# Kernel tuning notes

Hardware: AMD Instinct MI355X
Metric: run time of the kernel (lower is better)

The kernel has to match this reference:

```python
import math
import jax, jax.numpy as jnp
import numpy as np

DIM = 2048
HEAD_DIM = 64
N_HEADS = DIM // HEAD_DIM
BATCH = 4
SEQ = 1025  # 32*32 axial positions + 1 zero position
EPS = 1e-6


def make_theta(head_dim=HEAD_DIM, h=32, w=32):
    # freqs: geometric from pi to 10*pi, head_dim//4 of them
    n_freqs = head_dim // 4
    freqs = jnp.exp(jnp.linspace(math.log(math.pi), math.log(10 * math.pi), n_freqs))
    hp = jnp.linspace(-1.0, 1.0, h + 1)
    wp = jnp.linspace(-1.0, 1.0, w + 1)
    hp = (hp[:-1] + hp[1:]) / 2
    wp = (wp[:-1] + wp[1:]) / 2
    pos = jnp.stack(jnp.meshgrid(hp, wp, indexing='ij'), axis=-1).reshape(h * w, 2)
    pos = jnp.concatenate([jnp.zeros((1, 2)), pos], axis=0)  # [1025, 2]
    theta_h = pos[:, 0:1] * freqs  # [S, n_freqs]
    theta_w = pos[:, 1:2] * freqs
    return jnp.concatenate([theta_h, theta_w], axis=-1)  # [S, head_dim//2]


def rms_norm(x, scale, eps=EPS):
    mean_sq = jnp.mean(jnp.square(x.astype(jnp.float32)), axis=-1, keepdims=True)
    s = scale.astype(jnp.float32) * jax.lax.rsqrt(mean_sq + eps)
    return (x * s.astype(x.dtype)).astype(x.dtype)


def apply_rotary(x, theta):
    # x: [B, H, S, D], theta: [S, d] with 2*d <= D
    d = theta.shape[-1]
    x1, x2, x3 = x[..., :d], x[..., d:2 * d], x[..., 2 * d:]
    cos, sin = jnp.cos(theta), jnp.sin(theta)  # broadcast over B, H
    y1 = x1 * cos - x2 * sin
    y2 = x2 * cos + x1 * sin
    return jnp.concatenate([y1, y2, x3], axis=-1)


def setup_inputs() -> dict:
    key = jax.random.key(0)
    k1, k2, k3 = jax.random.split(key, 3)
    x = jax.random.normal(k1, (BATCH, SEQ, DIM), dtype=jnp.float32)
    scale = jnp.ones((DIM,), dtype=jnp.float32)
    w_qkv = jax.random.normal(k2, (3 * DIM, DIM), dtype=jnp.float32) * 0.02
    w_out = jax.random.normal(k3, (DIM, DIM), dtype=jnp.float32) * 0.02
    return {"x": x, "scale": scale, "w_qkv": w_qkv, "w_out": w_out}


def reference(x, scale, w_qkv, w_out):
    B, S, _ = x.shape
    skip = x
    h = rms_norm(x, scale)
    qkv = h @ w_qkv.T  # [B, S, 3*DIM]
    qkv = qkv.reshape(B, S, 3, N_HEADS, HEAD_DIM)
    qkv = jnp.transpose(qkv, (0, 3, 2, 1, 4))  # [B, H, 3, S, D]
    q, k, v = qkv[:, :, 0], qkv[:, :, 1], qkv[:, :, 2]
    theta = make_theta()[:S]
    q = apply_rotary(q, theta)
    k = apply_rotary(k, theta)
    scores = jnp.einsum('bhqd,bhkd->bhqk', q, k) / math.sqrt(HEAD_DIM)
    causal = jnp.tril(jnp.ones((S, S), dtype=bool))
    scores = jnp.where(causal, scores, jnp.finfo(scores.dtype).min)
    attn = jax.nn.softmax(scores, axis=-1)
    o = jnp.einsum('bhqk,bhkd->bhqd', attn, v)  # [B, H, S, D]
    o = jnp.transpose(o, (0, 2, 1, 3)).reshape(B, S, DIM)
    return o @ w_out.T + skip
```

## Files before the change

### kernel.cpp

```cpp
#include <hip/hip_runtime.h>
#include <hip/hip_bf16.h>
#include <cstdint>

#define SEQ   1025
#define SPAD  1088
#define DIM   2048
#define NQKV  6144
#define MROWS 4100
#define MPAD  4352
#define NH    32

typedef __attribute__((ext_vector_type(8))) short bf16x8;
typedef __attribute__((ext_vector_type(4))) short bf16x4;
typedef __attribute__((ext_vector_type(4))) float f32x4;

#define MFMA16x16(A,B,C) __builtin_amdgcn_mfma_f32_16x16x32_bf16(A,B,C,0,0,0)

static __device__ __forceinline__ float bf2f(short s) {
    union { unsigned int u; float f; } v;
    v.u = ((unsigned int)(unsigned short)s) << 16;
    return v.f;
}
static __device__ __forceinline__ short f2bf(float f) {
    union { float f; unsigned int u; } v; v.f = f;
    unsigned int r = v.u + 0x7fffu + ((v.u >> 16) & 1u);
    return (short)(r >> 16);
}

typedef __attribute__((address_space(1))) unsigned int u32g;
typedef __attribute__((address_space(3))) unsigned int u32l;
static __device__ __forceinline__ void gld_lds16(void* lds, const void* g) {
    __builtin_amdgcn_global_load_lds((const u32g*)(uintptr_t)g,
                                     (u32l*)(uintptr_t)lds, 16, 0, 0);
}

#define SBX() __builtin_amdgcn_sched_barrier(0)
#define PRIO(x) __builtin_amdgcn_s_setprio(x)

__global__ __launch_bounds__(256) void trig_k(float* __restrict__ cosT, float* __restrict__ sinT) {
    int i = blockIdx.x * 256 + threadIdx.x;
    if (i >= SEQ * 16) return;
    int s = i >> 4, f = i & 15;
    float ph = 0.f, pw = 0.f;
    if (s > 0) {
        int p = s - 1;
        ph = -1.f + ((p >> 5) + 0.5f) * 0.0625f;
        pw = -1.f + ((p & 31) + 0.5f) * 0.0625f;
    }
    double fr = 3.141592653589793 * exp((double)f * 0.15350567286626973);
    float th = (float)(ph * fr), tw = (float)(pw * fr);
    cosT[s*32 + f]      = cosf(th);
    sinT[s*32 + f]      = sinf(th);
    cosT[s*32 + 16 + f] = cosf(tw);
    sinT[s*32 + 16 + f] = sinf(tw);
}

__global__ __launch_bounds__(256) void rmsnorm_k(const float* __restrict__ x,
                                                 const float* __restrict__ sc,
                                                 short* __restrict__ h) {
    int row = blockIdx.x, t = threadIdx.x;
    short* hr = h + (size_t)row * DIM;
    if (row >= MROWS) {
        bf16x8 z = {};
        *(bf16x8*)(hr + t*8) = z;
        return;
    }
    const float4* xr = (const float4*)(x + (size_t)row * DIM);
    float4 a = xr[2*t], b = xr[2*t+1];
    float ss = a.x*a.x + a.y*a.y + a.z*a.z + a.w*a.w
             + b.x*b.x + b.y*b.y + b.z*b.z + b.w*b.w;
    #pragma unroll
    for (int off = 32; off; off >>= 1) ss += __shfl_xor(ss, off, 64);
    __shared__ float red[4];
    if ((t & 63) == 0) red[t >> 6] = ss;
    __syncthreads();
    float ms = (red[0]+red[1]+red[2]+red[3]) * (1.0f/2048.0f);
    float inv = rsqrtf(ms + 1e-6f);
    const float4* sr = (const float4*)sc;
    float4 s0 = sr[2*t], s1 = sr[2*t+1];
    bf16x8 o;
    o[0]=f2bf(a.x*(s0.x*inv)); o[1]=f2bf(a.y*(s0.y*inv));
    o[2]=f2bf(a.z*(s0.z*inv)); o[3]=f2bf(a.w*(s0.w*inv));
    o[4]=f2bf(b.x*(s1.x*inv)); o[5]=f2bf(b.y*(s1.y*inv));
    o[6]=f2bf(b.z*(s1.z*inv)); o[7]=f2bf(b.w*(s1.w*inv));
    *(bf16x8*)(hr + t*8) = o;
}

__global__ __launch_bounds__(256) void conv_k(const float* __restrict__ in, short* __restrict__ o, int n4) {
    int i = blockIdx.x * 256 + threadIdx.x;
    if (i >= n4) return;
    float4 v = ((const float4*)in)[i];
    bf16x4 r = { f2bf(v.x), f2bf(v.y), f2bf(v.z), f2bf(v.w) };
    *(bf16x4*)(o + (size_t)i*4) = r;
}

__global__ __launch_bounds__(512, 2) void gemm8p(const short* __restrict__ A,
                                                 const short* __restrict__ B,
                                                 short* __restrict__ C,
                                                 int N, int K, int nbm) {
    extern __shared__ char smem[];
    const int nwg = gridDim.x;
    const int cpx = nwg >> 3;
    const int bid = blockIdx.x;
    const int sid = (bid & 7) * cpx + (bid >> 3);
    const int bm = sid % nbm;
    const int bn = sid / nbm;

    const int t = threadIdx.x, w = t >> 6, l = t & 63;
    const int lr = l & 15, lg = l >> 4;
    const int wr = w >> 2, wc = w & 3;

    const short* Ab = A + (size_t)bm * 256 * K;
    const short* Bb = B + (size_t)bn * 256 * K;

    const int srow = t >> 3;
    const int scol = (((t & 7) ^ (srow & 7)) << 3);

    const int cs0 = (lg * 16) ^ ((lr & 7) << 4);
    const int cs1 = (64 + lg * 16) ^ ((lr & 7) << 4);
    const int aRowB = (wr * 128 + lr) * 128;
    const int bRowB = (wc * 64 + lr) * 128;

    f32x4 acc[8][4] = {};
    bf16x8 rA[4][2], rB[4][2];

#define STAGE8(kt, bb) do {                                                   \
    const int k0_ = (kt) * 64;                                                \
    _Pragma("unroll")                                                         \
    for (int c = 0; c < 4; ++c) {                                             \
        gld_lds16(smem + (bb)*65536 + c*8192 + (w<<10),                       \
                  Ab + (size_t)(c*64 + srow) * K + k0_ + scol);               \
        gld_lds16(smem + (bb)*65536 + 32768 + c*8192 + (w<<10),               \
                  Bb + (size_t)(c*64 + srow) * K + k0_ + scol);               \
    }                                                                         \
} while (0)

#define READ_A8(bb, h) do {                                                   \
    const char* p_ = smem + (bb)*65536 + aRowB + (h)*8192;                    \
    _Pragma("unroll")                                                         \
    for (int am = 0; am < 4; ++am) {                                          \
        rA[am][0] = *(const bf16x8*)(p_ + am*2048 + cs0);                     \
        rA[am][1] = *(const bf16x8*)(p_ + am*2048 + cs1);                     \
    }                                                                         \
} while (0)

#define READ_B4(bb, np) do {                                                  \
    const char* p_ = smem + (bb)*65536 + 32768 + bRowB + (np)*4096;           \
    _Pragma("unroll")                                                         \
    for (int nn = 0; nn < 2; ++nn) {                                          \
        rB[(np)*2+nn][0] = *(const bf16x8*)(p_ + nn*2048 + cs0);              \
        rB[(np)*2+nn][1] = *(const bf16x8*)(p_ + nn*2048 + cs1);              \
    }                                                                         \
} while (0)

#define MF_Q(h, nh) do {                                                      \
    _Pragma("unroll")                                                         \
    for (int am = 0; am < 4; ++am)                                            \
    _Pragma("unroll")                                                         \
    for (int nn = 0; nn < 2; ++nn) {                                          \
        acc[(h)*4+am][(nh)*2+nn] =                                            \
            MFMA16x16(rA[am][0], rB[(nh)*2+nn][0], acc[(h)*4+am][(nh)*2+nn]); \
        acc[(h)*4+am][(nh)*2+nn] =                                            \
            MFMA16x16(rA[am][1], rB[(nh)*2+nn][1], acc[(h)*4+am][(nh)*2+nn]); \
    }                                                                         \
} while (0)

#define PH_COMPUTE(h, nh) do {                                                \
    SBX(); __builtin_amdgcn_s_barrier();                                      \
    asm volatile("s_waitcnt lgkmcnt(0)" ::: "memory"); SBX();                 \
    PRIO(1); MF_Q(h, nh); PRIO(0); SBX();                                     \
    __builtin_amdgcn_s_barrier(); SBX();                                      \
} while (0)

    STAGE8(0, 0);
    STAGE8(1, 1);
    asm volatile("s_waitcnt vmcnt(8)" ::: "memory"); SBX();
    __builtin_amdgcn_s_barrier(); SBX();

    const int NT2 = K / 128;
    for (int it = 0; it < NT2; ++it) {
        const bool more = (it < NT2 - 1);
        READ_A8(0, 0); READ_B4(0, 0); PH_COMPUTE(0, 0);
        READ_B4(0, 1);                PH_COMPUTE(0, 1);
        READ_A8(0, 1);                PH_COMPUTE(1, 1);
        if (more) STAGE8(2*it + 2, 0);
        SBX(); __builtin_amdgcn_s_barrier(); SBX();
        PRIO(1); MF_Q(1, 0); PRIO(0); SBX();
        if (more) { asm volatile("s_waitcnt vmcnt(8)" ::: "memory"); }
        else      { asm volatile("s_waitcnt vmcnt(0)" ::: "memory"); }
        SBX(); __builtin_amdgcn_s_barrier(); SBX();
        READ_A8(1, 0); READ_B4(1, 0); PH_COMPUTE(0, 0);
        READ_B4(1, 1);                PH_COMPUTE(0, 1);
        READ_A8(1, 1);                PH_COMPUTE(1, 1);
        if (more) STAGE8(2*it + 3, 1);
        SBX(); __builtin_amdgcn_s_barrier(); SBX();
        PRIO(1); MF_Q(1, 0); PRIO(0); SBX();
        if (more) { asm volatile("s_waitcnt vmcnt(8)" ::: "memory"); SBX(); }
        __builtin_amdgcn_s_barrier(); SBX();
    }

    #pragma unroll
    for (int m = 0; m < 8; ++m) {
        const int row0 = bm*256 + wr*128 + m*16 + lg*4;
        #pragma unroll
        for (int n = 0; n < 4; ++n) {
            const int col = bn*256 + wc*64 + n*16 + lr;
            #pragma unroll
            for (int r = 0; r < 4; ++r)
                C[(size_t)(row0 + r) * N + col] = f2bf(acc[m][n][r]);
        }
    }
#undef STAGE8
#undef READ_A8
#undef READ_B4
#undef MF_Q
#undef PH_COMPUTE
}

__global__ __launch_bounds__(256) void gemm_bt(const short* __restrict__ A,
                                               const short* __restrict__ B,
                                               float* __restrict__ C,
                                               const float* __restrict__ skip,
                                               int N, int K, int nbm) {
    __shared__ short As[128*32];
    __shared__ short Bs[128*32];
    const int nwg = gridDim.x;
    const int cpx = nwg >> 3;
    const int bid = blockIdx.x;
    const int sid = (bid & 7) * cpx + (bid >> 3);
    const int bm = sid % nbm, bn = sid / nbm;
    const int t = threadIdx.x;
    const int w = t >> 6, l = t & 63;
    const int lr = l & 15, lg = l >> 4;
    const int wr = w >> 1, wc = w & 1;
    const short* Ab = A + (size_t)bm * 128 * K;
    const short* Bb = B + (size_t)bn * 128 * K;

    f32x4 acc[4][4] = {};

    const int c1 = t + 256;
    const int ar0 = t >> 2,  ac0 = (t & 3) * 8;
    const int ar1 = c1 >> 2, ac1 = (c1 & 3) * 8;

    for (int k0 = 0; k0 < K; k0 += 32) {
        gld_lds16((char*)As + (w << 10),        Ab + (size_t)ar0 * K + k0 + ac0);
        gld_lds16((char*)As + 4096 + (w << 10), Ab + (size_t)ar1 * K + k0 + ac1);
        gld_lds16((char*)Bs + (w << 10),        Bb + (size_t)ar0 * K + k0 + ac0);
        gld_lds16((char*)Bs + 4096 + (w << 10), Bb + (size_t)ar1 * K + k0 + ac1);
        __syncthreads();
        bf16x8 af[4], bfv[4];
        #pragma unroll
        for (int m = 0; m < 4; ++m)
            af[m] = *(const bf16x8*)(As + (wr*64 + m*16 + lr)*32 + lg*8);
        #pragma unroll
        for (int n = 0; n < 4; ++n)
            bfv[n] = *(const bf16x8*)(Bs + (wc*64 + n*16 + lr)*32 + lg*8);
        #pragma unroll
        for (int m = 0; m < 4; ++m)
            #pragma unroll
            for (int n = 0; n < 4; ++n)
                acc[m][n] = MFMA16x16(af[m], bfv[n], acc[m][n]);
        __syncthreads();
    }

    #pragma unroll
    for (int m = 0; m < 4; ++m) {
        const int row0 = bm*128 + wr*64 + m*16 + lg*4;
        #pragma unroll
        for (int n = 0; n < 4; ++n) {
            const int col = bn*128 + wc*64 + n*16 + lr;
            #pragma unroll
            for (int r = 0; r < 4; ++r) {
                const int row = row0 + r;
                if (row < MROWS)
                    C[(size_t)row * N + col] =
                        acc[m][n][r] + skip[(size_t)row * N + col];
            }
        }
    }
}

__global__ __launch_bounds__(256) void rearrange_k(const short* __restrict__ qkv,
        const float* __restrict__ cosT, const float* __restrict__ sinT,
        short* __restrict__ kr, short* __restrict__ vt) {
    int bid = blockIdx.x;
    int bh = bid / 17, st = bid % 17;
    int b = bh >> 5, hh = bh & 31;
    int s0 = st * 64;
    int t = threadIdx.x;
    __shared__ short vs[64][68];
    #pragma unroll
    for (int i = 0; i < 8; ++i) {
        int task = t + i*256;
        int sl = task >> 5, p = task & 31;
        int s = s0 + sl;
        float y1 = 0.f, y2 = 0.f;
        if (s < SEQ) {
            const short* src = qkv + (size_t)(b*SEQ + s)*NQKV + DIM + hh*64;
            float x1 = bf2f(src[p]), x2 = bf2f(src[32+p]);
            float c = cosT[s*32+p], sn = sinT[s*32+p];
            y1 = x1*c - x2*sn;
            y2 = x2*c + x1*sn;
        }
        short* dst = kr + ((size_t)bh*SPAD + s)*64;
        dst[p]    = f2bf(y1);
        dst[32+p] = f2bf(y2);
    }
    #pragma unroll
    for (int i = 0; i < 16; ++i) {
        int task = t + i*256;
        int sl = task >> 6, d = task & 63;
        int s = s0 + sl;
        short v = 0;
        if (s < SEQ) v = qkv[(size_t)(b*SEQ + s)*NQKV + 2*DIM + hh*64 + d];
        vs[sl][d] = v;
    }
    __syncthreads();
    #pragma unroll
    for (int i = 0; i < 16; ++i) {
        int task = t + i*256;
        int d = task >> 6, sl = task & 63;
        vt[((size_t)bh*64 + d)*SPAD + s0 + sl] = vs[sl][d];
    }
}

__global__ __launch_bounds__(256) void attn_k(const short* __restrict__ qkv,
        const short* __restrict__ kr, const short* __restrict__ vt,
        const float* __restrict__ cosT, const float* __restrict__ sinT,
        short* __restrict__ ob) {
    const int nwg = gridDim.x;
    const int cpx = nwg >> 3;
    const int bid = blockIdx.x;
    const int sid = (bid & 7) * cpx + (bid >> 3);
    const int bh = sid / 17;
    const int q0 = (sid % 17) * 64;
    const int b = bh >> 5, hh = bh & 31;
    const int t = threadIdx.x, w = t >> 6, l = t & 63;
    const int lr = l & 15, lg = l >> 4;

    __shared__ short Ks[32*64];
    __shared__ short Vts[64*32];

    const int qrow = q0 + w*16 + lr;
    const int qc = qrow < SEQ ? qrow : SEQ-1;
    const short* qsrc = qkv + (size_t)(b*SEQ + qc)*NQKV + hh*64;
    bf16x8 xlo = *(const bf16x8*)(qsrc + lg*8);
    bf16x8 xhi = *(const bf16x8*)(qsrc + 32 + lg*8);
    const float4* cp = (const float4*)(cosT + qc*32 + lg*8);
    const float4* sp = (const float4*)(sinT + qc*32 + lg*8);
    float cc[8], sn[8];
    { float4 u = cp[0], v2 = cp[1];
      cc[0]=u.x; cc[1]=u.y; cc[2]=u.z; cc[3]=u.w;
      cc[4]=v2.x; cc[5]=v2.y; cc[6]=v2.z; cc[7]=v2.w; }
    { float4 u = sp[0], v2 = sp[1];
      sn[0]=u.x; sn[1]=u.y; sn[2]=u.z; sn[3]=u.w;
      sn[4]=v2.x; sn[5]=v2.y; sn[6]=v2.z; sn[7]=v2.w; }
    bf16x8 qf0, qf1;
    #pragma unroll
    for (int j = 0; j < 8; ++j) {
        float x1 = bf2f(xlo[j]), x2 = bf2f(xhi[j]);
        qf0[j] = f2bf(x1*cc[j] - x2*sn[j]);
        qf1[j] = f2bf(x2*cc[j] + x1*sn[j]);
    }

    f32x4 oacc[4] = {};
    float mrun = -1e30f, lrun = 0.f;
    const int ntile = min((q0 + 64 + 31) >> 5, 33);
    const float SC = 0.125f * 1.4426950408889634f;

    const short* kbase = kr + (size_t)bh * SPAD * 64;
    const short* vbase = vt + (size_t)bh * 64 * SPAD;

    const int skrow = t >> 3, skslot = t & 7;
    const int svrow = t >> 2, svslot = t & 3;

    for (int kt = 0; kt < ntile; ++kt) {
        const int kv0 = kt * 32;
        gld_lds16((char*)Ks + (w<<10),
                  (const char*)(kbase + (size_t)(kv0 + skrow)*64) + ((skslot ^ (skrow & 7)) << 4));
        gld_lds16((char*)Vts + (w<<10),
                  (const char*)(vbase + (size_t)svrow*SPAD + kv0) + ((svslot ^ ((svrow>>1) & 3)) << 4));
        __syncthreads();

        f32x4 st0 = {}, st1 = {};
        {
            const int krow = lr;
            const int swz = (krow & 7) << 4;
            const char* kp = (const char*)Ks + krow*128;
            bf16x8 a0 = *(const bf16x8*)(kp + ((lg*16) ^ swz));
            bf16x8 a1 = *(const bf16x8*)(kp + ((64 + lg*16) ^ swz));
            st0 = MFMA16x16(a0, qf0, st0);
            st0 = MFMA16x16(a1, qf1, st0);
        }
        {
            const int krow = 16 + lr;
            const int swz = (krow & 7) << 4;
            const char* kp = (const char*)Ks + krow*128;
            bf16x8 a0 = *(const bf16x8*)(kp + ((lg*16) ^ swz));
            bf16x8 a1 = *(const bf16x8*)(kp + ((64 + lg*16) ^ swz));
            st1 = MFMA16x16(a0, qf0, st1);
            st1 = MFMA16x16(a1, qf1, st1);
        }

        float sv[8];
        float tmax = -1e30f;
        #pragma unroll
        for (int r = 0; r < 4; ++r) {
            int kv = kv0 + lg*4 + r;
            float v = st0[r] * SC;
            v = (kv <= qrow && kv < SEQ) ? v : -1e30f;
            sv[r] = v; tmax = fmaxf(tmax, v);
        }
        #pragma unroll
        for (int r = 0; r < 4; ++r) {
            int kv = kv0 + 16 + lg*4 + r;
            float v = st1[r] * SC;
            v = (kv <= qrow && kv < SEQ) ? v : -1e30f;
            sv[4+r] = v; tmax = fmaxf(tmax, v);
        }
        tmax = fmaxf(tmax, __shfl_xor(tmax, 16, 64));
        tmax = fmaxf(tmax, __shfl_xor(tmax, 32, 64));
        float mnew = fmaxf(mrun, tmax);
        float alpha = exp2f(mrun - mnew);
        float psum = 0.f;
        bf16x8 pf;
        #pragma unroll
        for (int i2 = 0; i2 < 8; ++i2) {
            float p = exp2f(sv[i2] - mnew);
            psum += p;
            pf[i2] = f2bf(p);
        }
        psum += __shfl_xor(psum, 16, 64);
        psum += __shfl_xor(psum, 32, 64);
        lrun = lrun * alpha + psum;
        mrun = mnew;
        #pragma unroll
        for (int df = 0; df < 4; ++df) {
            oacc[df][0] *= alpha; oacc[df][1] *= alpha;
            oacc[df][2] *= alpha; oacc[df][3] *= alpha;
        }
        #pragma unroll
        for (int df = 0; df < 4; ++df) {
            const int vrow = df*16 + lr;
            const int swz = ((vrow >> 1) & 3) << 4;
            const char* vp = (const char*)Vts + vrow*64;
            bf16x4 v0 = *(const bf16x4*)(vp + ((lg*8) ^ swz));
            bf16x4 v1 = *(const bf16x4*)(vp + ((32 + lg*8) ^ swz));
            bf16x8 vf;
            vf[0]=v0[0]; vf[1]=v0[1]; vf[2]=v0[2]; vf[3]=v0[3];
            vf[4]=v1[0]; vf[5]=v1[1]; vf[6]=v1[2]; vf[7]=v1[3];
            oacc[df] = MFMA16x16(vf, pf, oacc[df]);
        }
        __syncthreads();
    }

    if (qrow < SEQ) {
        float inv = 1.0f / lrun;
        short* orow = ob + (size_t)(b*SEQ + qrow)*DIM + hh*64;
        #pragma unroll
        for (int df = 0; df < 4; ++df) {
            bf16x4 ov = { f2bf(oacc[df][0]*inv), f2bf(oacc[df][1]*inv),
                          f2bf(oacc[df][2]*inv), f2bf(oacc[df][3]*inv) };
            *(bf16x4*)(orow + df*16 + lg*4) = ov;
        }
    }
}

extern "C" void kernel_launch(void* const* d_in, const int* in_sizes, int n_in,
                              void* d_out, int out_size, void* d_ws, size_t ws_size,
                              hipStream_t stream) {
    const float* x     = (const float*)d_in[0];
    const float* scale = (const float*)d_in[1];
    const float* w_qkv = (const float*)d_in[2];
    const float* w_out = (const float*)d_in[3];
    float* out = (float*)d_out;

    char* ws = (char*)d_ws;
    size_t off = 0;
    auto alloc = [&](size_t bytes) -> char* {
        char* p = ws + off;
        off += (bytes + 255) & ~(size_t)255;
        return p;
    };
    float* cosT  = (float*)alloc((size_t)SEQ*32*4);
    float* sinT  = (float*)alloc((size_t)SEQ*32*4);
    short* h_b   = (short*)alloc((size_t)MPAD*DIM*2);
    short* wq_b  = (short*)alloc((size_t)NQKV*DIM*2);
    short* wo_b  = (short*)alloc((size_t)DIM*DIM*2);
    short* qkv_b = (short*)alloc((size_t)MPAD*NQKV*2);
    short* k_r   = (short*)alloc((size_t)128*SPAD*64*2);
    short* vt    = (short*)alloc((size_t)128*SPAD*64*2);
    short* o_b   = h_b;

    hipFuncSetAttribute((const void*)gemm8p,
                        hipFuncAttributeMaxDynamicSharedMemorySize, 131072);

    trig_k<<<65, 256, 0, stream>>>(cosT, sinT);
    rmsnorm_k<<<MPAD, 256, 0, stream>>>(x, scale, h_b);
    conv_k<<<(NQKV*DIM/4 + 255)/256, 256, 0, stream>>>(w_qkv, wq_b, NQKV*DIM/4);
    conv_k<<<(DIM*DIM/4 + 255)/256, 256, 0, stream>>>(w_out, wo_b, DIM*DIM/4);
    gemm8p<<<(MPAD/256)*(NQKV/256), 512, 131072, stream>>>(h_b, wq_b, qkv_b, NQKV, DIM, MPAD/256);
    rearrange_k<<<128*17, 256, 0, stream>>>(qkv_b, cosT, sinT, k_r, vt);
    attn_k<<<17*128, 256, 0, stream>>>(qkv_b, k_r, vt, cosT, sinT, o_b);
    gemm_bt<<<(MPAD/128)*(DIM/128), 256, 0, stream>>>(o_b, wo_b, out, x, DIM, DIM, MPAD/128);
}
```

Baseline: 467.2 us.

## Reuse 256x256 pipelined GEMM for output projection, widen attention KV tiles, split staging

The simple 128x128 output-projection GEMM is dropped in favour of the 256x256 pipelined gemm8p kernel, templated with a residual-add fp32 epilogue. The gemm8p main loop now issues its global-to-LDS prefetch in two parts between MFMA phases and drops several barriers and waits. The attention kernel processes 64 keys per tile instead of 32, with larger shared K/V buffers, halving loop iterations and synchronisations. The output GEMM gets only 136 large workgroups, which may under-fill the GPU.

```diff
diff --git a/kernel.cpp b/kernel.cpp
--- a/kernel.cpp
+++ b/kernel.cpp
@@ -94,9 +94,11 @@
     *(bf16x4*)(o + (size_t)i*4) = r;
 }
 
+template<int EPI>
 __global__ __launch_bounds__(512, 2) void gemm8p(const short* __restrict__ A,
                                                  const short* __restrict__ B,
-                                                 short* __restrict__ C,
+                                                 void* __restrict__ C,
+                                                 const float* __restrict__ skip,
                                                  int N, int K, int nbm) {
     extern __shared__ char smem[];
     const int nwg = gridDim.x;
@@ -135,6 +137,26 @@
     }                                                                         \
 } while (0)
 
+#define STAGE_P2(kt, bb) do {                                                 \
+    const int k0_ = (kt) * 64;                                                \
+    gld_lds16(smem + (bb)*65536 + 0*8192 + (w<<10),                           \
+              Ab + (size_t)(0*64 + srow) * K + k0_ + scol);                   \
+    gld_lds16(smem + (bb)*65536 + 2*8192 + (w<<10),                           \
+              Ab + (size_t)(2*64 + srow) * K + k0_ + scol);                   \
+    _Pragma("unroll")                                                         \
+    for (int c = 0; c < 4; ++c)                                               \
+        gld_lds16(smem + (bb)*65536 + 32768 + c*8192 + (w<<10),               \
+                  Bb + (size_t)(c*64 + srow) * K + k0_ + scol);               \
+} while (0)
+
+#define STAGE_P3(kt, bb) do {                                                 \
+    const int k0_ = (kt) * 64;                                                \
+    gld_lds16(smem + (bb)*65536 + 1*8192 + (w<<10),                           \
+              Ab + (size_t)(1*64 + srow) * K + k0_ + scol);                   \
+    gld_lds16(smem + (bb)*65536 + 3*8192 + (w<<10),                           \
+              Ab + (size_t)(3*64 + srow) * K + k0_ + scol);                   \
+} while (0)
+
 #define READ_A8(bb, h) do {                                                   \
     const char* p_ = smem + (bb)*65536 + aRowB + (h)*8192;                    \
     _Pragma("unroll")                                                         \
@@ -165,38 +187,39 @@
     }                                                                         \
 } while (0)
 
-#define PH_COMPUTE(h, nh) do {                                                \
-    SBX(); __builtin_amdgcn_s_barrier();                                      \
-    asm volatile("s_waitcnt lgkmcnt(0)" ::: "memory"); SBX();                 \
-    PRIO(1); MF_Q(h, nh); PRIO(0); SBX();                                     \
-    __builtin_amdgcn_s_barrier(); SBX();                                      \
-} while (0)
+#define BAR() do { SBX(); __builtin_amdgcn_s_barrier(); } while (0)
 
     STAGE8(0, 0);
     STAGE8(1, 1);
     asm volatile("s_waitcnt vmcnt(8)" ::: "memory"); SBX();
-    __builtin_amdgcn_s_barrier(); SBX();
+    __builtin_amdgcn_s_barrier();
 
     const int NT2 = K / 128;
     for (int it = 0; it < NT2; ++it) {
         const bool more = (it < NT2 - 1);
-        READ_A8(0, 0); READ_B4(0, 0); PH_COMPUTE(0, 0);
-        READ_B4(0, 1);                PH_COMPUTE(0, 1);
-        READ_A8(0, 1);                PH_COMPUTE(1, 1);
-        if (more) STAGE8(2*it + 2, 0);
-        SBX(); __builtin_amdgcn_s_barrier(); SBX();
-        PRIO(1); MF_Q(1, 0); PRIO(0); SBX();
+        READ_A8(0, 0); READ_B4(0, 0);
+        PRIO(1); MF_Q(0, 0); PRIO(0); BAR();
+        READ_B4(0, 1);
+        PRIO(1); MF_Q(0, 1); PRIO(0); BAR();
+        if (more) STAGE_P2(2*it + 2, 0);
+        READ_A8(0, 1);
+        PRIO(1); MF_Q(1, 1); PRIO(0); BAR();
+        if (more) STAGE_P3(2*it + 2, 0);
+        PRIO(1); MF_Q(1, 0); PRIO(0);
         if (more) { asm volatile("s_waitcnt vmcnt(8)" ::: "memory"); }
         else      { asm volatile("s_waitcnt vmcnt(0)" ::: "memory"); }
-        SBX(); __builtin_amdgcn_s_barrier(); SBX();
-        READ_A8(1, 0); READ_B4(1, 0); PH_COMPUTE(0, 0);
-        READ_B4(1, 1);                PH_COMPUTE(0, 1);
-        READ_A8(1, 1);                PH_COMPUTE(1, 1);
-        if (more) STAGE8(2*it + 3, 1);
-        SBX(); __builtin_amdgcn_s_barrier(); SBX();
-        PRIO(1); MF_Q(1, 0); PRIO(0); SBX();
-        if (more) { asm volatile("s_waitcnt vmcnt(8)" ::: "memory"); SBX(); }
-        __builtin_amdgcn_s_barrier(); SBX();
+        BAR();
+        READ_A8(1, 0); READ_B4(1, 0);
+        PRIO(1); MF_Q(0, 0); PRIO(0); BAR();
+        READ_B4(1, 1);
+        PRIO(1); MF_Q(0, 1); PRIO(0); BAR();
+        if (more) STAGE_P2(2*it + 3, 1);
+        READ_A8(1, 1);
+        PRIO(1); MF_Q(1, 1); PRIO(0); BAR();
+        if (more) STAGE_P3(2*it + 3, 1);
+        PRIO(1); MF_Q(1, 0); PRIO(0);
+        if (more) { asm volatile("s_waitcnt vmcnt(8)" ::: "memory"); }
+        BAR();
     }
 
     #pragma unroll
@@ -206,78 +229,25 @@
         for (int n = 0; n < 4; ++n) {
             const int col = bn*256 + wc*64 + n*16 + lr;
             #pragma unroll
-            for (int r = 0; r < 4; ++r)
-                C[(size_t)(row0 + r) * N + col] = f2bf(acc[m][n][r]);
+            for (int r = 0; r < 4; ++r) {
+                const int row = row0 + r;
+                if constexpr (EPI == 0) {
+                    ((short*)C)[(size_t)row * N + col] = f2bf(acc[m][n][r]);
+                } else {
+                    if (row < MROWS)
+                        ((float*)C)[(size_t)row * N + col] =
+                            acc[m][n][r] + skip[(size_t)row * N + col];
+                }
+            }
         }
     }
 #undef STAGE8
+#undef STAGE_P2
+#undef STAGE_P3
 #undef READ_A8
 #undef READ_B4
 #undef MF_Q
-#undef PH_COMPUTE
-}
-
-__global__ __launch_bounds__(256) void gemm_bt(const short* __restrict__ A,
-                                               const short* __restrict__ B,
-                                               float* __restrict__ C,
-                                               const float* __restrict__ skip,
-                                               int N, int K, int nbm) {
-    __shared__ short As[128*32];
-    __shared__ short Bs[128*32];
-    const int nwg = gridDim.x;
-    const int cpx = nwg >> 3;
-    const int bid = blockIdx.x;
-    const int sid = (bid & 7) * cpx + (bid >> 3);
-    const int bm = sid % nbm, bn = sid / nbm;
-    const int t = threadIdx.x;
-    const int w = t >> 6, l = t & 63;
-    const int lr = l & 15, lg = l >> 4;
-    const int wr = w >> 1, wc = w & 1;
-    const short* Ab = A + (size_t)bm * 128 * K;
-    const short* Bb = B + (size_t)bn * 128 * K;
-
-    f32x4 acc[4][4] = {};
-
-    const int c1 = t + 256;
-    const int ar0 = t >> 2,  ac0 = (t & 3) * 8;
-    const int ar1 = c1 >> 2, ac1 = (c1 & 3) * 8;
-
-    for (int k0 = 0; k0 < K; k0 += 32) {
-        gld_lds16((char*)As + (w << 10),        Ab + (size_t)ar0 * K + k0 + ac0);
-        gld_lds16((char*)As + 4096 + (w << 10), Ab + (size_t)ar1 * K + k0 + ac1);
-        gld_lds16((char*)Bs + (w << 10),        Bb + (size_t)ar0 * K + k0 + ac0);
-        gld_lds16((char*)Bs + 4096 + (w << 10), Bb + (size_t)ar1 * K + k0 + ac1);
-        __syncthreads();
-        bf16x8 af[4], bfv[4];
-        #pragma unroll
-        for (int m = 0; m < 4; ++m)
-            af[m] = *(const bf16x8*)(As + (wr*64 + m*16 + lr)*32 + lg*8);
-        #pragma unroll
-        for (int n = 0; n < 4; ++n)
-            bfv[n] = *(const bf16x8*)(Bs + (wc*64 + n*16 + lr)*32 + lg*8);
-        #pragma unroll
-        for (int m = 0; m < 4; ++m)
-            #pragma unroll
-            for (int n = 0; n < 4; ++n)
-                acc[m][n] = MFMA16x16(af[m], bfv[n], acc[m][n]);
-        __syncthreads();
-    }
-
-    #pragma unroll
-    for (int m = 0; m < 4; ++m) {
-        const int row0 = bm*128 + wr*64 + m*16 + lg*4;
-        #pragma unroll
-        for (int n = 0; n < 4; ++n) {
-            const int col = bn*128 + wc*64 + n*16 + lr;
-            #pragma unroll
-            for (int r = 0; r < 4; ++r) {
-                const int row = row0 + r;
-                if (row < MROWS)
-                    C[(size_t)row * N + col] =
-                        acc[m][n][r] + skip[(size_t)row * N + col];
-            }
-        }
-    }
+#undef BAR
 }
 
 __global__ __launch_bounds__(256) void rearrange_k(const short* __restrict__ qkv,
@@ -333,13 +303,14 @@
     const int bid = blockIdx.x;
     const int sid = (bid & 7) * cpx + (bid >> 3);
     const int bh = sid / 17;
-    const int q0 = (sid % 17) * 64;
+    const int qt = sid % 17;
+    const int q0 = qt * 64;
     const int b = bh >> 5, hh = bh & 31;
     const int t = threadIdx.x, w = t >> 6, l = t & 63;
     const int lr = l & 15, lg = l >> 4;
 
-    __shared__ short Ks[32*64];
-    __shared__ short Vts[64*32];
+    __shared__ short Ks[64*64];
+    __shared__ short Vts[64*64];
 
     const int qrow = q0 + w*16 + lr;
     const int qc = qrow < SEQ ? qrow : SEQ-1;
@@ -365,70 +336,64 @@
 
     f32x4 oacc[4] = {};
     float mrun = -1e30f, lrun = 0.f;
-    const int ntile = min((q0 + 64 + 31) >> 5, 33);
+    const int ntile = qt + 1;
     const float SC = 0.125f * 1.4426950408889634f;
 
-    const short* kbase = kr + (size_t)bh * SPAD * 64;
-    const short* vbase = vt + (size_t)bh * 64 * SPAD;
-
-    const int skrow = t >> 3, skslot = t & 7;
-    const int svrow = t >> 2, svslot = t & 3;
+    const char* kbase = (const char*)(kr + (size_t)bh * SPAD * 64);
+    const char* vbase = (const char*)(vt + (size_t)bh * 64 * SPAD);
+    const int srow8 = l >> 3;
+    const int sslotB = ((l & 7) ^ srow8) << 4;
+    const int swz = (lr & 7) << 4;
 
     for (int kt = 0; kt < ntile; ++kt) {
-        const int kv0 = kt * 32;
-        gld_lds16((char*)Ks + (w<<10),
-                  (const char*)(kbase + (size_t)(kv0 + skrow)*64) + ((skslot ^ (skrow & 7)) << 4));
-        gld_lds16((char*)Vts + (w<<10),
-                  (const char*)(vbase + (size_t)svrow*SPAD + kv0) + ((svslot ^ ((svrow>>1) & 3)) << 4));
+        const int kv0 = kt * 64;
+        gld_lds16((char*)Ks + w*2048,
+                  kbase + (size_t)(kv0 + w*16 + srow8)*128 + sslotB);
+        gld_lds16((char*)Ks + w*2048 + 1024,
+                  kbase + (size_t)(kv0 + w*16 + 8 + srow8)*128 + sslotB);
+        gld_lds16((char*)Vts + w*2048,
+                  vbase + (size_t)(w*16 + srow8)*(SPAD*2) + (size_t)kv0*2 + sslotB);
+        gld_lds16((char*)Vts + w*2048 + 1024,
+                  vbase + (size_t)(w*16 + 8 + srow8)*(SPAD*2) + (size_t)kv0*2 + sslotB);
         __syncthreads();
 
-        f32x4 st0 = {}, st1 = {};
-        {
-            const int krow = lr;
-            const int swz = (krow & 7) << 4;
-            const char* kp = (const char*)Ks + krow*128;
+        f32x4 st[4];
+        #pragma unroll
+        for (int f = 0; f < 4; ++f) {
+            const char* kp = (const char*)Ks + (f*16 + lr)*128;
             bf16x8 a0 = *(const bf16x8*)(kp + ((lg*16) ^ swz));
             bf16x8 a1 = *(const bf16x8*)(kp + ((64 + lg*16) ^ swz));
-            st0 = MFMA16x16(a0, qf0, st0);
-            st0 = MFMA16x16(a1, qf1, st0);
-        }
-        {
-            const int krow = 16 + lr;
-            const int swz = (krow & 7) << 4;
-            const char* kp = (const char*)Ks + krow*128;
-            bf16x8 a0 = *(const bf16x8*)(kp + ((lg*16) ^ swz));
-            bf16x8 a1 = *(const bf16x8*)(kp + ((64 + lg*16) ^ swz));
-            st1 = MFMA16x16(a0, qf0, st1);
-            st1 = MFMA16x16(a1, qf1, st1);
-        }
-
-        float sv[8];
+            f32x4 z = {};
+            z = MFMA16x16(a0, qf0, z);
+            st[f] = MFMA16x16(a1, qf1, z);
+        }
+
+        float pv[16];
         float tmax = -1e30f;
         #pragma unroll
+        for (int f = 0; f < 4; ++f)
+        #pragma unroll
         for (int r = 0; r < 4; ++r) {
-            int kv = kv0 + lg*4 + r;
-            float v = st0[r] * SC;
+            int kv = kv0 + f*16 + lg*4 + r;
+            float v = st[f][r] * SC;
             v = (kv <= qrow && kv < SEQ) ? v : -1e30f;
-            sv[r] = v; tmax = fmaxf(tmax, v);
-        }
-        #pragma unroll
-        for (int r = 0; r < 4; ++r) {
-            int kv = kv0 + 16 + lg*4 + r;
-            float v = st1[r] * SC;
-            v = (kv <= qrow && kv < SEQ) ? v : -1e30f;
-            sv[4+r] = v; tmax = fmaxf(tmax, v);
+            pv[f*4+r] = v; tmax = fmaxf(tmax, v);
         }
         tmax = fmaxf(tmax, __shfl_xor(tmax, 16, 64));
         tmax = fmaxf(tmax, __shfl_xor(tmax, 32, 64));
         float mnew = fmaxf(mrun, tmax);
         float alpha = exp2f(mrun - mnew);
         float psum = 0.f;
-        bf16x8 pf;
-        #pragma unroll
-        for (int i2 = 0; i2 < 8; ++i2) {
-            float p = exp2f(sv[i2] - mnew);
-            psum += p;
-            pf[i2] = f2bf(p);
+        bf16x8 pf0, pf1;
+        #pragma unroll
+        for (int j = 0; j < 4; ++j) {
+            float p0 = exp2f(pv[0*4+j] - mnew);
+            float p1 = exp2f(pv[1*4+j] - mnew);
+            float p2 = exp2f(pv[2*4+j] - mnew);
+            float p3 = exp2f(pv[3*4+j] - mnew);
+            psum += (p0 + p1) + (p2 + p3);
+            pf0[j] = f2bf(p0); pf0[4+j] = f2bf(p1);
+            pf1[j] = f2bf(p2); pf1[4+j] = f2bf(p3);
         }
         psum += __shfl_xor(psum, 16, 64);
         psum += __shfl_xor(psum, 32, 64);
@@ -441,15 +406,18 @@
         }
         #pragma unroll
         for (int df = 0; df < 4; ++df) {
-            const int vrow = df*16 + lr;
-            const int swz = ((vrow >> 1) & 3) << 4;
-            const char* vp = (const char*)Vts + vrow*64;
+            const char* vp = (const char*)Vts + (df*16 + lr)*128;
             bf16x4 v0 = *(const bf16x4*)(vp + ((lg*8) ^ swz));
             bf16x4 v1 = *(const bf16x4*)(vp + ((32 + lg*8) ^ swz));
-            bf16x8 vf;
-            vf[0]=v0[0]; vf[1]=v0[1]; vf[2]=v0[2]; vf[3]=v0[3];
-            vf[4]=v1[0]; vf[5]=v1[1]; vf[6]=v1[2]; vf[7]=v1[3];
-            oacc[df] = MFMA16x16(vf, pf, oacc[df]);
+            bf16x4 v2 = *(const bf16x4*)(vp + ((64 + lg*8) ^ swz));
+            bf16x4 v3 = *(const bf16x4*)(vp + ((96 + lg*8) ^ swz));
+            bf16x8 vf0, vf1;
+            vf0[0]=v0[0]; vf0[1]=v0[1]; vf0[2]=v0[2]; vf0[3]=v0[3];
+            vf0[4]=v1[0]; vf0[5]=v1[1]; vf0[6]=v1[2]; vf0[7]=v1[3];
+            vf1[0]=v2[0]; vf1[1]=v2[1]; vf1[2]=v2[2]; vf1[3]=v2[3];
+            vf1[4]=v3[0]; vf1[5]=v3[1]; vf1[6]=v3[2]; vf1[7]=v3[3];
+            oacc[df] = MFMA16x16(vf0, pf0, oacc[df]);
+            oacc[df] = MFMA16x16(vf1, pf1, oacc[df]);
         }
         __syncthreads();
     }
@@ -492,15 +460,17 @@
     short* vt    = (short*)alloc((size_t)128*SPAD*64*2);
     short* o_b   = h_b;
 
-    hipFuncSetAttribute((const void*)gemm8p,
+    hipFuncSetAttribute((const void*)gemm8p<0>,
+                        hipFuncAttributeMaxDynamicSharedMemorySize, 131072);
+    hipFuncSetAttribute((const void*)gemm8p<1>,
                         hipFuncAttributeMaxDynamicSharedMemorySize, 131072);
 
     trig_k<<<65, 256, 0, stream>>>(cosT, sinT);
     rmsnorm_k<<<MPAD, 256, 0, stream>>>(x, scale, h_b);
     conv_k<<<(NQKV*DIM/4 + 255)/256, 256, 0, stream>>>(w_qkv, wq_b, NQKV*DIM/4);
     conv_k<<<(DIM*DIM/4 + 255)/256, 256, 0, stream>>>(w_out, wo_b, DIM*DIM/4);
-    gemm8p<<<(MPAD/256)*(NQKV/256), 512, 131072, stream>>>(h_b, wq_b, qkv_b, NQKV, DIM, MPAD/256);
+    gemm8p<0><<<(MPAD/256)*(NQKV/256), 512, 131072, stream>>>(h_b, wq_b, qkv_b, nullptr, NQKV, DIM, MPAD/256);
     rearrange_k<<<128*17, 256, 0, stream>>>(qkv_b, cosT, sinT, k_r, vt);
     attn_k<<<17*128, 256, 0, stream>>>(qkv_b, k_r, vt, cosT, sinT, o_b);
-    gemm_bt<<<(MPAD/128)*(DIM/128), 256, 0, stream>>>(o_b, wo_b, out, x, DIM, DIM, MPAD/128);
-}
+    gemm8p<1><<<(MPAD/256)*(DIM/256), 512, 131072, stream>>>(o_b, wo_b, out, x, DIM, DIM, MPAD/256);
+}
```

New measurement: 436.5 us. 1.07x faster.
